# Kernel tuning notes

Measured on AMD Instinct MI355X. Metric: run time of the kernel, lower is better.

Reference implementation:

```python
import jax, jax.numpy as jnp
import numpy as np

THRESHOLD = 33.33  # torch forward default

def setup_inputs() -> dict:
    key = jax.random.key(0)
    k1, k2 = jax.random.split(key)
    source_pc = jax.random.normal(k1, (2, 16384, 3), dtype=jnp.float32)
    target_pc = jax.random.normal(k2, (2, 16384, 3), dtype=jnp.float32)
    return {"source_pc": source_pc, "target_pc": target_pc}

def _pairwise_dist(x, y):
    # Euclidean cdist via the matmul expansion (same math as torch.cdist p=2).
    # x: [B, N, D], y: [B, M, D] -> [B, N, M]
    x2 = jnp.sum(x * x, axis=-1)              # [B, N]
    y2 = jnp.sum(y * y, axis=-1)              # [B, M]
    xy = jnp.einsum('bnd,bmd->bnm', x, y)     # [B, N, M]
    d2 = x2[:, :, None] + y2[None if False else slice(None), None, :] - 2.0 * xy
    d2 = x2[:, :, None] + y2[:, None, :] - 2.0 * xy
    return jnp.sqrt(jnp.maximum(d2, 0.0))

def reference(source_pc, target_pc):
    dist = _pairwise_dist(source_pc.astype(jnp.float32), target_pc.astype(jnp.float32))
    dist1 = jnp.minimum(jnp.min(dist, axis=2), THRESHOLD)  # [B, N] clamped
    dist2 = jnp.minimum(jnp.min(dist, axis=1), THRESHOLD)  # [B, M] clamped
    d1 = jnp.mean(dist1, axis=-1)
    d2 = jnp.mean(dist2, axis=-1)
    return (d1 + d2) / 2.0  # bidirectional=True default -> [B]
```

## Files before the change

### kernel.cpp

```cpp
#include <hip/hip_runtime.h>

#define NPTS 16384
#define TH 33.33f

typedef __attribute__((ext_vector_type(8)))  __bf16 bf16x8;
typedef __attribute__((ext_vector_type(16))) float  f32x16;

__device__ __forceinline__ unsigned short f2bf(float x) {
    unsigned u = __float_as_uint(x);
    u += 0x7FFFu + ((u >> 16) & 1u);
    return (unsigned short)(u >> 16);
}
__device__ __forceinline__ float bf2f(unsigned short h) {
    return __uint_as_float(((unsigned)h) << 16);
}

union U8 { unsigned short s[8]; uint4 v; };


__global__ __launch_bounds__(256) void prep_kernel(const float* __restrict__ src,
        const float* __restrict__ tgt, unsigned short* __restrict__ mats,
        float* __restrict__ harr, unsigned int* __restrict__ d2min,
        float* __restrict__ out) {
    int t = blockIdx.x * 256 + threadIdx.x;
    if (t < 2) out[t] = 0.0f;
    d2min[t] = 0x7F800000u;
    int b = t >> 15, set = (t >> 14) & 1, p = t & (NPTS - 1);
    const float* pc = (set ? tgt : src) + ((size_t)b * NPTS + p) * 3;
    float x = pc[0], y = pc[1], z = pc[2];
    float hp = 0.5f * fmaf(z, z, fmaf(y, y, x * x));
    harr[(b * 2 + set) * NPTS + p] = hp;
    unsigned short xh = f2bf(x), yh = f2bf(y), zh = f2bf(z);
    unsigned short xl = f2bf(x - bf2f(xh)), yl = f2bf(y - bf2f(yh)), zl = f2bf(z - bf2f(zh));
    float r = hp;
    unsigned short h0 = f2bf(r); r -= bf2f(h0);
    unsigned short h1 = f2bf(r); r -= bf2f(h1);
    unsigned short h2 = f2bf(r);
    unsigned short n0 = h0 ^ 0x8000, n1 = h1 ^ 0x8000, n2 = h2 ^ 0x8000;
    const unsigned short one = 0x3F80;
    U8 a0, a1, c0, c1;
    a0.s[0]=xh; a0.s[1]=yh; a0.s[2]=zh; a0.s[3]=xl; a0.s[4]=yl; a0.s[5]=zl; a0.s[6]=xh; a0.s[7]=yh;
    a1.s[0]=zh; a1.s[1]=one; a1.s[2]=one; a1.s[3]=one; a1.s[4]=0; a1.s[5]=0; a1.s[6]=0; a1.s[7]=0;
    c0.s[0]=xh; c0.s[1]=yh; c0.s[2]=zh; c0.s[3]=xh; c0.s[4]=yh; c0.s[5]=zh; c0.s[6]=xl; c0.s[7]=yl;
    c1.s[0]=zl; c1.s[1]=n0; c1.s[2]=n1; c1.s[3]=n2; c1.s[4]=0; c1.s[5]=0; c1.s[6]=0; c1.s[7]=0;
    size_t tile = p >> 5; int ll = p & 31;
    size_t iA = ((size_t)(b * 4 + set))     * NPTS * 16 + tile * 512 + ll * 8;
    size_t iB = ((size_t)(b * 4 + 2 + set)) * NPTS * 16 + tile * 512 + ll * 8;
    *(uint4*)(mats + iA)       = a0.v;
    *(uint4*)(mats + iA + 256) = a1.v;
    *(uint4*)(mats + iB)       = c0.v;
    *(uint4*)(mats + iB + 256) = c1.v;
}

#define FOLD(MM, AA) { \
    f32x16 t0 = __builtin_amdgcn_mfma_f32_32x32x16_bf16(AA, q0, zc, 0, 0, 0); \
    f32x16 t1 = __builtin_amdgcn_mfma_f32_32x32x16_bf16(AA, q1, zc, 0, 0, 0); \
    _Pragma("unroll") for (int j = 0; j < 16; j++) MM[j] = fmaxf(fmaxf(t0[j], t1[j]), MM[j]); }

#define EPILOG(MM, P) { \
    float* sc = &scratch[wave][0][0]; \
    _Pragma("unroll") for (int j = 0; j < 16; j++) { \
        int r0 = (j & 3) + 8 * (j >> 2) + 4 * g; sc[r0 * 33 + cc] = MM[j]; } \
    __syncthreads(); \
    const float* sr = &scratch[wave][0][0] + cc * 33 + g * 16; \
    float mx = -3.0e38f; \
    _Pragma("unroll") for (int k = 0; k < 16; k++) mx = fmaxf(mx, sr[k]); \
    mx = fmaxf(mx, __shfl_xor(mx, 32, 64)); \
    if (lane < 32) { \
        int grow = (rt0 + P) * 32 + lane; \
        float hq = hqbase[grow]; \
        float d2 = 2.0f * (hq - mx); \
        float d = fminf(sqrtf(fmaxf(d2, 0.0f)), TH); \
        atomicMin(&dmin[grow], __float_as_uint(d)); } \
    __syncthreads(); }

__global__ __launch_bounds__(256, 3) void gemm_kernel(const unsigned short* __restrict__ mats,
        const float* __restrict__ harr, unsigned int* __restrict__ d2min) {
    const int db = blockIdx.y, dir = db >> 1, b = db & 1;
    const int rowblock = blockIdx.x >> 3, seg = blockIdx.x & 7;
    const int tid = threadIdx.x, wave = tid >> 6, lane = tid & 63;
    const int g = lane >> 5, cc = lane & 31;
    const unsigned short* Am = mats + ((size_t)(b * 4 + dir))     * NPTS * 16;
    const unsigned short* Bm = mats + ((size_t)(b * 4 + 3 - dir)) * NPTS * 16;

    const int rt0 = rowblock * 16 + wave * 4;
    bf16x8 a0 = *(const bf16x8*)(Am + (size_t)(rt0 + 0) * 512 + lane * 8);
    bf16x8 a1 = *(const bf16x8*)(Am + (size_t)(rt0 + 1) * 512 + lane * 8);
    bf16x8 a2 = *(const bf16x8*)(Am + (size_t)(rt0 + 2) * 512 + lane * 8);
    bf16x8 a3 = *(const bf16x8*)(Am + (size_t)(rt0 + 3) * 512 + lane * 8);

    __shared__ alignas(16) unsigned short sbuf[8192];
    __shared__ float scratch[4][32][33];

    f32x16 m0 = -3.0e38f, m1 = -3.0e38f, m2 = -3.0e38f, m3 = -3.0e38f;
    const f32x16 zc = 0.0f;

    const unsigned short* Bseg = Bm + (size_t)seg * 64 * 512;

    for (int c = 0; c < 4; ++c) {
        const char* gbase = (const char*)(Bseg + (size_t)c * 16 * 512);
#pragma unroll
        for (int i = 0; i < 4; i++) {
            __builtin_amdgcn_global_load_lds(
                (const __attribute__((address_space(1))) unsigned int*)(gbase + i * 4096 + tid * 16),
                (__attribute__((address_space(3))) unsigned int*)((char*)sbuf + i * 4096 + tid * 16),
                16, 0, 0);
        }
        __syncthreads();
#pragma unroll 1
        for (int pt = 0; pt < 8; ++pt) {
            bf16x8 q0 = *(const bf16x8*)(sbuf + pt * 1024 + lane * 8);
            bf16x8 q1 = *(const bf16x8*)(sbuf + pt * 1024 + 512 + lane * 8);
            FOLD(m0, a0)
            FOLD(m1, a1)
            FOLD(m2, a2)
            FOLD(m3, a3)
        }
        __syncthreads();
    }

    const float* hqbase = harr + (size_t)(b * 2 + dir) * NPTS;
    unsigned int* dmin = d2min + (size_t)db * NPTS;
    EPILOG(m0, 0)
    EPILOG(m1, 1)
    EPILOG(m2, 2)
    EPILOG(m3, 3)
}

__global__ __launch_bounds__(256) void merge_kernel(const unsigned int* __restrict__ d2min,
                                                    float* __restrict__ out) {
    int i = blockIdx.x * 256 + threadIdx.x;
    float a0 = __uint_as_float(d2min[0 * NPTS + i]) + __uint_as_float(d2min[2 * NPTS + i]);
    float a1 = __uint_as_float(d2min[1 * NPTS + i]) + __uint_as_float(d2min[3 * NPTS + i]);
#pragma unroll
    for (int off = 32; off > 0; off >>= 1) {
        a0 += __shfl_down(a0, off, 64);
        a1 += __shfl_down(a1, off, 64);
    }
    __shared__ float w0[4], w1[4];
    int wv = threadIdx.x >> 6;
    if ((threadIdx.x & 63) == 0) { w0[wv] = a0; w1[wv] = a1; }
    __syncthreads();
    if (threadIdx.x == 0) {
        const float inv = 1.0f / (2.0f * NPTS);
        atomicAdd(&out[0], (w0[0] + w0[1] + w0[2] + w0[3]) * inv);
        atomicAdd(&out[1], (w1[0] + w1[1] + w1[2] + w1[3]) * inv);
    }
}

extern "C" void kernel_launch(void* const* d_in, const int* in_sizes, int n_in,
                              void* d_out, int out_size, void* d_ws, size_t ws_size,
                              hipStream_t stream) {
    const float* src = (const float*)d_in[0];
    const float* tgt = (const float*)d_in[1];
    float* out = (float*)d_out;
    unsigned short* mats = (unsigned short*)d_ws;
    float* harr = (float*)((char*)d_ws + 4194304);
    unsigned int* d2min = (unsigned int*)((char*)d_ws + 4194304 + 262144);

    prep_kernel<<<256, 256, 0, stream>>>(src, tgt, mats, harr, d2min, out);
    gemm_kernel<<<dim3(256, 4), 256, 0, stream>>>(mats, harr, d2min);
    merge_kernel<<<64, 256, 0, stream>>>(d2min, out);
}
```

Before: 102.9 us.

## Fuse bf16 split-encoding prep into chamfer GEMM kernel and drop atomics

Removes the separate prep kernel by building the A fragments and the per-chunk B tiles directly from the float point clouds inside the MFMA kernel, using a double-buffered LDS ping-pong so the next chunk's encoding overlaps the current chunk's MFMAs. The atomicMin into a global min array is replaced by writing per-segment partial minima to a workspace, which a reworked 2-block merge kernel reduces with min over segments and then a sum. This saves one launch and the round trip of the encoded matrices through memory. In exchange each block redundantly recomputes the encodings, the B loads are uncoalesced stride-3 float reads, and the merge now runs on only two blocks.

```diff
diff --git a/kernel.cpp b/kernel.cpp
--- a/kernel.cpp
+++ b/kernel.cpp
@@ -15,136 +15,135 @@
     return __uint_as_float(((unsigned)h) << 16);
 }
 
-union U8 { unsigned short s[8]; uint4 v; };
+union UV { uint4 v; bf16x8 h; unsigned short s[8]; };
 
 
-__global__ __launch_bounds__(256) void prep_kernel(const float* __restrict__ src,
-        const float* __restrict__ tgt, unsigned short* __restrict__ mats,
-        float* __restrict__ harr, unsigned int* __restrict__ d2min,
-        float* __restrict__ out) {
-    int t = blockIdx.x * 256 + threadIdx.x;
-    if (t < 2) out[t] = 0.0f;
-    d2min[t] = 0x7F800000u;
-    int b = t >> 15, set = (t >> 14) & 1, p = t & (NPTS - 1);
-    const float* pc = (set ? tgt : src) + ((size_t)b * NPTS + p) * 3;
-    float x = pc[0], y = pc[1], z = pc[2];
-    float hp = 0.5f * fmaf(z, z, fmaf(y, y, x * x));
-    harr[(b * 2 + set) * NPTS + p] = hp;
-    unsigned short xh = f2bf(x), yh = f2bf(y), zh = f2bf(z);
-    unsigned short xl = f2bf(x - bf2f(xh)), yl = f2bf(y - bf2f(yh)), zl = f2bf(z - bf2f(zh));
-    float r = hp;
-    unsigned short h0 = f2bf(r); r -= bf2f(h0);
-    unsigned short h1 = f2bf(r); r -= bf2f(h1);
-    unsigned short h2 = f2bf(r);
-    unsigned short n0 = h0 ^ 0x8000, n1 = h1 ^ 0x8000, n2 = h2 ^ 0x8000;
-    const unsigned short one = 0x3F80;
-    U8 a0, a1, c0, c1;
-    a0.s[0]=xh; a0.s[1]=yh; a0.s[2]=zh; a0.s[3]=xl; a0.s[4]=yl; a0.s[5]=zl; a0.s[6]=xh; a0.s[7]=yh;
-    a1.s[0]=zh; a1.s[1]=one; a1.s[2]=one; a1.s[3]=one; a1.s[4]=0; a1.s[5]=0; a1.s[6]=0; a1.s[7]=0;
-    c0.s[0]=xh; c0.s[1]=yh; c0.s[2]=zh; c0.s[3]=xh; c0.s[4]=yh; c0.s[5]=zh; c0.s[6]=xl; c0.s[7]=yl;
-    c1.s[0]=zl; c1.s[1]=n0; c1.s[2]=n1; c1.s[3]=n2; c1.s[4]=0; c1.s[5]=0; c1.s[6]=0; c1.s[7]=0;
-    size_t tile = p >> 5; int ll = p & 31;
-    size_t iA = ((size_t)(b * 4 + set))     * NPTS * 16 + tile * 512 + ll * 8;
-    size_t iB = ((size_t)(b * 4 + 2 + set)) * NPTS * 16 + tile * 512 + ll * 8;
-    *(uint4*)(mats + iA)       = a0.v;
-    *(uint4*)(mats + iA + 256) = a1.v;
-    *(uint4*)(mats + iB)       = c0.v;
-    *(uint4*)(mats + iB + 256) = c1.v;
-}
-
-#define FOLD(MM, AA) { \
+#define FOLD2(MM, AA) { \
     f32x16 t0 = __builtin_amdgcn_mfma_f32_32x32x16_bf16(AA, q0, zc, 0, 0, 0); \
     f32x16 t1 = __builtin_amdgcn_mfma_f32_32x32x16_bf16(AA, q1, zc, 0, 0, 0); \
     _Pragma("unroll") for (int j = 0; j < 16; j++) MM[j] = fmaxf(fmaxf(t0[j], t1[j]), MM[j]); }
 
+#define PREP_CHUNK(CC, BUF) { \
+    unsigned short* lb = (unsigned short*)(smem + (BUF) * 16384); \
+    _Pragma("unroll") for (int u = 0; u < 2; u++) { \
+        int k = tid * 2 + u; \
+        int gp = seg * 2048 + (CC) * 512 + k; \
+        float x = pp[gp * 3 + 0], y = pp[gp * 3 + 1], z = pp[gp * 3 + 2]; \
+        float hp = 0.5f * fmaf(z, z, fmaf(y, y, x * x)); \
+        unsigned short xh = f2bf(x), yh = f2bf(y), zh = f2bf(z); \
+        unsigned short xl = f2bf(x - bf2f(xh)), yl = f2bf(y - bf2f(yh)), zl = f2bf(z - bf2f(zh)); \
+        float rr = hp; \
+        unsigned short h0 = f2bf(rr); rr -= bf2f(h0); \
+        unsigned short h1 = f2bf(rr); rr -= bf2f(h1); \
+        unsigned short h2 = f2bf(rr); \
+        UV c0, c1; \
+        c0.s[0]=xh; c0.s[1]=yh; c0.s[2]=zh; c0.s[3]=xh; c0.s[4]=yh; c0.s[5]=zh; c0.s[6]=xl; c0.s[7]=yl; \
+        c1.s[0]=zl; c1.s[1]=(unsigned short)(h0^0x8000); c1.s[2]=(unsigned short)(h1^0x8000); \
+        c1.s[3]=(unsigned short)(h2^0x8000); c1.s[4]=0; c1.s[5]=0; c1.s[6]=0; c1.s[7]=0; \
+        int t = k >> 5, pos = k & 31; \
+        *(uint4*)(lb + t * 512 + pos * 8)       = c0.v; \
+        *(uint4*)(lb + t * 512 + 256 + pos * 8) = c1.v; } }
+
 #define EPILOG(MM, P) { \
-    float* sc = &scratch[wave][0][0]; \
+    float* sc = scratch + wave * 1056; \
     _Pragma("unroll") for (int j = 0; j < 16; j++) { \
         int r0 = (j & 3) + 8 * (j >> 2) + 4 * g; sc[r0 * 33 + cc] = MM[j]; } \
     __syncthreads(); \
-    const float* sr = &scratch[wave][0][0] + cc * 33 + g * 16; \
+    const float* sr = sc + cc * 33 + g * 16; \
     float mx = -3.0e38f; \
     _Pragma("unroll") for (int k = 0; k < 16; k++) mx = fmaxf(mx, sr[k]); \
     mx = fmaxf(mx, __shfl_xor(mx, 32, 64)); \
     if (lane < 32) { \
-        int grow = (rt0 + P) * 32 + lane; \
-        float hq = hqbase[grow]; \
-        float d2 = 2.0f * (hq - mx); \
+        float d2 = 2.0f * (hq[P] - mx); \
         float d = fminf(sqrtf(fmaxf(d2, 0.0f)), TH); \
-        atomicMin(&dmin[grow], __float_as_uint(d)); } \
+        dst[wave * 128 + (P) * 32 + lane] = d; } \
     __syncthreads(); }
 
-__global__ __launch_bounds__(256, 3) void gemm_kernel(const unsigned short* __restrict__ mats,
-        const float* __restrict__ harr, unsigned int* __restrict__ d2min) {
+__global__ __launch_bounds__(256, 3) void chamfer_kernel(
+        const float* __restrict__ src, const float* __restrict__ tgt,
+        float* __restrict__ d2part)
+{
     const int db = blockIdx.y, dir = db >> 1, b = db & 1;
     const int rowblock = blockIdx.x >> 3, seg = blockIdx.x & 7;
     const int tid = threadIdx.x, wave = tid >> 6, lane = tid & 63;
     const int g = lane >> 5, cc = lane & 31;
-    const unsigned short* Am = mats + ((size_t)(b * 4 + dir))     * NPTS * 16;
-    const unsigned short* Bm = mats + ((size_t)(b * 4 + 3 - dir)) * NPTS * 16;
+    const float* qp = (dir == 0 ? src : tgt) + (size_t)b * NPTS * 3;
+    const float* pp = (dir == 0 ? tgt : src) + (size_t)b * NPTS * 3;
+    const unsigned short one = 0x3F80;
+
+    __shared__ alignas(16) unsigned char smem[32768];
+    float* scratch = (float*)smem;
 
     const int rt0 = rowblock * 16 + wave * 4;
-    bf16x8 a0 = *(const bf16x8*)(Am + (size_t)(rt0 + 0) * 512 + lane * 8);
-    bf16x8 a1 = *(const bf16x8*)(Am + (size_t)(rt0 + 1) * 512 + lane * 8);
-    bf16x8 a2 = *(const bf16x8*)(Am + (size_t)(rt0 + 2) * 512 + lane * 8);
-    bf16x8 a3 = *(const bf16x8*)(Am + (size_t)(rt0 + 3) * 512 + lane * 8);
-
-    __shared__ alignas(16) unsigned short sbuf[8192];
-    __shared__ float scratch[4][32][33];
+    bf16x8 afrag[4]; float hq[4];
+#pragma unroll
+    for (int i = 0; i < 4; i++) {
+        int r = (rt0 + i) * 32 + cc;
+        float x = qp[r * 3 + 0], y = qp[r * 3 + 1], z = qp[r * 3 + 2];
+        hq[i] = 0.5f * fmaf(z, z, fmaf(y, y, x * x));
+        unsigned short xh = f2bf(x), yh = f2bf(y), zh = f2bf(z);
+        unsigned short xl = f2bf(x - bf2f(xh)), yl = f2bf(y - bf2f(yh)), zl = f2bf(z - bf2f(zh));
+        UV f0, f1, rv;
+        f0.s[0]=xh; f0.s[1]=yh; f0.s[2]=zh; f0.s[3]=xl; f0.s[4]=yl; f0.s[5]=zl; f0.s[6]=xh; f0.s[7]=yh;
+        f1.s[0]=zh; f1.s[1]=one; f1.s[2]=one; f1.s[3]=one; f1.s[4]=0; f1.s[5]=0; f1.s[6]=0; f1.s[7]=0;
+        rv.v = g ? f1.v : f0.v;
+        afrag[i] = rv.h;
+    }
 
     f32x16 m0 = -3.0e38f, m1 = -3.0e38f, m2 = -3.0e38f, m3 = -3.0e38f;
     const f32x16 zc = 0.0f;
 
-    const unsigned short* Bseg = Bm + (size_t)seg * 64 * 512;
-
+    PREP_CHUNK(0, 0)
+    __syncthreads();
+#pragma unroll 1
     for (int c = 0; c < 4; ++c) {
-        const char* gbase = (const char*)(Bseg + (size_t)c * 16 * 512);
-#pragma unroll
-        for (int i = 0; i < 4; i++) {
-            __builtin_amdgcn_global_load_lds(
-                (const __attribute__((address_space(1))) unsigned int*)(gbase + i * 4096 + tid * 16),
-                (__attribute__((address_space(3))) unsigned int*)((char*)sbuf + i * 4096 + tid * 16),
-                16, 0, 0);
-        }
-        __syncthreads();
+        if (c < 3) { PREP_CHUNK(c + 1, (c + 1) & 1) }
+        const unsigned short* bb = (const unsigned short*)(smem + (c & 1) * 16384);
 #pragma unroll 1
         for (int pt = 0; pt < 8; ++pt) {
-            bf16x8 q0 = *(const bf16x8*)(sbuf + pt * 1024 + lane * 8);
-            bf16x8 q1 = *(const bf16x8*)(sbuf + pt * 1024 + 512 + lane * 8);
-            FOLD(m0, a0)
-            FOLD(m1, a1)
-            FOLD(m2, a2)
-            FOLD(m3, a3)
+            bf16x8 q0 = *(const bf16x8*)(bb + pt * 1024 + lane * 8);
+            bf16x8 q1 = *(const bf16x8*)(bb + pt * 1024 + 512 + lane * 8);
+            FOLD2(m0, afrag[0])
+            FOLD2(m1, afrag[1])
+            FOLD2(m2, afrag[2])
+            FOLD2(m3, afrag[3])
         }
         __syncthreads();
     }
 
-    const float* hqbase = harr + (size_t)(b * 2 + dir) * NPTS;
-    unsigned int* dmin = d2min + (size_t)db * NPTS;
+    float* dst = d2part + (((size_t)(db * 32 + rowblock)) * 8 + seg) * 512;
     EPILOG(m0, 0)
     EPILOG(m1, 1)
     EPILOG(m2, 2)
     EPILOG(m3, 3)
 }
 
-__global__ __launch_bounds__(256) void merge_kernel(const unsigned int* __restrict__ d2min,
-                                                    float* __restrict__ out) {
-    int i = blockIdx.x * 256 + threadIdx.x;
-    float a0 = __uint_as_float(d2min[0 * NPTS + i]) + __uint_as_float(d2min[2 * NPTS + i]);
-    float a1 = __uint_as_float(d2min[1 * NPTS + i]) + __uint_as_float(d2min[3 * NPTS + i]);
+__global__ __launch_bounds__(1024) void merge_kernel(const float* __restrict__ d2part,
+                                                     float* __restrict__ out) {
+    const int b = blockIdx.x;
+    const int tid = threadIdx.x;
+    float s = 0.0f;
 #pragma unroll
-    for (int off = 32; off > 0; off >>= 1) {
-        a0 += __shfl_down(a0, off, 64);
-        a1 += __shfl_down(a1, off, 64);
+    for (int pass = 0; pass < 2; pass++) {
+        const float* base = d2part + (size_t)(pass * 2 + b) * 32 * 8 * 512;
+        for (int r = tid; r < NPTS; r += 1024) {
+            const float* p = base + (size_t)(r >> 9) * 4096 + (r & 511);
+            float m = p[0];
+#pragma unroll
+            for (int sgi = 1; sgi < 8; sgi++) m = fminf(m, p[sgi * 512]);
+            s += m;
+        }
     }
-    __shared__ float w0[4], w1[4];
-    int wv = threadIdx.x >> 6;
-    if ((threadIdx.x & 63) == 0) { w0[wv] = a0; w1[wv] = a1; }
+#pragma unroll
+    for (int off = 32; off > 0; off >>= 1) s += __shfl_down(s, off, 64);
+    __shared__ float w[16];
+    if ((tid & 63) == 0) w[tid >> 6] = s;
     __syncthreads();
-    if (threadIdx.x == 0) {
-        const float inv = 1.0f / (2.0f * NPTS);
-        atomicAdd(&out[0], (w0[0] + w0[1] + w0[2] + w0[3]) * inv);
-        atomicAdd(&out[1], (w1[0] + w1[1] + w1[2] + w1[3]) * inv);
+    if (tid == 0) {
+        float t = 0.0f;
+#pragma unroll
+        for (int i = 0; i < 16; i++) t += w[i];
+        out[b] = t * (1.0f / (2.0f * NPTS));
     }
 }
 
@@ -154,11 +153,8 @@
     const float* src = (const float*)d_in[0];
     const float* tgt = (const float*)d_in[1];
     float* out = (float*)d_out;
-    unsigned short* mats = (unsigned short*)d_ws;
-    float* harr = (float*)((char*)d_ws + 4194304);
-    unsigned int* d2min = (unsigned int*)((char*)d_ws + 4194304 + 262144);
+    float* d2part = (float*)d_ws;
 
-    prep_kernel<<<256, 256, 0, stream>>>(src, tgt, mats, harr, d2min, out);
-    gemm_kernel<<<dim3(256, 4), 256, 0, stream>>>(mats, harr, d2min);
-    merge_kernel<<<64, 256, 0, stream>>>(d2min, out);
+    chamfer_kernel<<<dim3(256, 4), 256, 0, stream>>>(src, tgt, d2part);
+    merge_kernel<<<2, 1024, 0, stream>>>(d2part, out);
 }
```

After: 108.6 us. 1.06x slower.
